# Kernel tuning notes

Measured on AMD Instinct MI355X. Metric: run time of the kernel, lower is better.

The kernel has to match this reference:

```python
import jax, jax.numpy as jnp
import numpy as np

N_DRUG, N_MICROBE = 1500, 1572
N = N_DRUG + N_MICROBE          # 3072 nodes
F_IN = 1546                     # raw feature dim (fc1: 1546 -> 256)
D0 = 256                        # GCN input dim after fc1
H1 = H2 = 128                   # GCN hidden dims (H1 + H2 = 256)
B = 16384                       # number of (left,right) query pairs


def _sym_norm(A):
    # D^{-1/2} A D^{-1/2} (no self loops), zeros kept for isolated nodes
    deg = A.sum(axis=1)
    d = jnp.where(deg > 0, jax.lax.rsqrt(deg), 0.0)
    return A * d[:, None] * d[None, :]


def _compute_inf(adj, L):
    # dl.compute_inf: L-hop influence = L-th power of sym-normalized adjacency
    An = _sym_norm(adj)
    M = An
    for _ in range(L - 1):
        M = M @ An
    return M


def _gcn_norm(W):
    # GCNConv normalization: add self loops (weight 1), sym-normalize by weighted degree
    Ahat = W + jnp.eye(W.shape[0], dtype=W.dtype)
    deg = Ahat.sum(axis=1)
    d = jnp.where(deg > 0, jax.lax.rsqrt(deg), 0.0)
    return Ahat * d[:, None] * d[None, :]


def _glorot(key, shape):
    return jax.random.normal(key, shape, dtype=jnp.float32) / np.sqrt(shape[0])


def setup_inputs() -> dict:
    key = jax.random.key(0)
    ks = jax.random.split(key, 24)
    u = jax.random.uniform(ks[0], (N, N), dtype=jnp.float32)
    w = jax.random.uniform(ks[1], (N, N), dtype=jnp.float32)
    adj = jnp.where(u < 0.01, w, 0.0)
    adj = jnp.maximum(adj, adj.T)
    X = jax.random.normal(ks[2], (N, F_IN), dtype=jnp.float32)
    left = jax.random.randint(ks[3], (B,), 0, N)
    right = jax.random.randint(ks[4], (B,), 0, N)
    return dict(
        left=left, right=right, X=X, adj=adj, threshold=jnp.float32(1e-4),
        W_fc1=_glorot(ks[5], (F_IN, D0)), b_fc1=jnp.zeros((D0,), jnp.float32),
        Wg1=_glorot(ks[6], (D0, H1)), bg1=jnp.zeros((H1,), jnp.float32),
        Wg2=_glorot(ks[7], (H1, H2)), bg2=jnp.zeros((H2,), jnp.float32),
        Wg3=_glorot(ks[8], (D0, H1)), bg3=jnp.zeros((H1,), jnp.float32),
        Wg4=_glorot(ks[9], (H1, H2)), bg4=jnp.zeros((H2,), jnp.float32),
        Wg5=_glorot(ks[10], (D0, H1)), bg5=jnp.zeros((H1,), jnp.float32),
        Wg6=_glorot(ks[11], (H1, H2)), bg6=jnp.zeros((H2,), jnp.float32),
        cnn_k=jax.random.normal(ks[12], (1, 3, 3, 3), dtype=jnp.float32) * 0.1,
        cnn_b=jnp.zeros((1,), jnp.float32),
        W_a=_glorot(ks[13], (2 * (H1 + H2), 64)), b_a=jnp.zeros((64,), jnp.float32),
        W_b=_glorot(ks[14], (64, 2)), b_b=jnp.zeros((2,), jnp.float32),
    )


def reference(left, right, X, adj, threshold,
              W_fc1, b_fc1, Wg1, bg1, Wg2, bg2, Wg3, bg3, Wg4, bg4,
              Wg5, bg5, Wg6, bg6, cnn_k, cnn_b, W_a, b_a, W_b, b_b):
    X0 = jax.nn.relu(X @ W_fc1 + b_fc1)  # fc1: [N, 1546] -> [N, 256]

    def branch(mask_src, Wa, ba, Wb, bb):
        # dynamically thresholded edges carry the ORIGINAL adj weights
        Wadj = jnp.where(mask_src > threshold, adj, 0.0)
        An = _gcn_norm(Wadj)                       # [N, N]
        e1 = jax.nn.relu(An @ (X0 @ Wa) + ba)      # GCNConv 1
        e2 = jax.nn.relu(An @ (e1 @ Wb) + bb)      # GCNConv 2
        return jnp.concatenate([e1, e2], axis=1)   # [N, 256]

    emb_l2 = branch(_compute_inf(adj, 2), Wg1, bg1, Wg2, bg2)
    emb_l1 = branch(_compute_inf(adj, 1), Wg3, bg3, Wg4, bg4)
    emb_l0 = branch(adj, Wg5, bg5, Wg6, bg6)

    emb = jnp.stack([emb_l0, emb_l1, emb_l2], axis=0)[None]  # [1, 3, N, 256]
    conv = jax.lax.conv_general_dilated(
        emb, cnn_k, window_strides=(1, 1), padding=[(2, 2), (2, 2)],
        rhs_dilation=(2, 2), dimension_numbers=('NCHW', 'OIHW', 'NCHW'))
    emb_all = conv[0, 0] + cnn_b[0]                # [N, 256]

    pair = jnp.concatenate([emb_all[left], emb_all[right]], axis=1)  # [B, 512]
    h = jax.nn.relu(pair @ W_a + b_a)              # dropout is identity at eval
    logits = h @ W_b + b_b                         # [B, 2]
    return logits, emb_all
```

## Files before the change

kernel.cpp:

```cpp
#include <hip/hip_runtime.h>

#define NN 3072
#define FIN 1546
#define KP 1568
#define MAXR 192

#define XS4_BLOCKS (NN * KP / 1024)
#define WSPLIT_BLOCKS (256 * KP / 256)
#define WG_BLOCKS 704
#define CSR_BLOCKS (NN / 4)
#define FC1_BLOCKS (NN / 16 * 4)

typedef __attribute__((ext_vector_type(8))) __bf16 bf16x8;
typedef __attribute__((ext_vector_type(4))) __bf16 bf16x4;
typedef __attribute__((ext_vector_type(4))) float f32x4;

__global__ __launch_bounds__(256) void prep_k(const float* __restrict__ adj,
                                              int* __restrict__ cols, float* __restrict__ vals,
                                              int* __restrict__ cnt, float* __restrict__ dvec,
                                              const float* __restrict__ X,
                                              __bf16* __restrict__ Xh, __bf16* __restrict__ Xl,
                                              const float* __restrict__ W,
                                              __bf16* __restrict__ WhT, __bf16* __restrict__ WlT,
                                              const float* __restrict__ Wga0,
                                              const float* __restrict__ Wga1,
                                              const float* __restrict__ Wga2,
                                              const float* __restrict__ Wgb0,
                                              const float* __restrict__ Wgb1,
                                              const float* __restrict__ Wgb2,
                                              const float* __restrict__ Wa,
                                              __bf16* __restrict__ WgaTh, __bf16* __restrict__ WgaTl,
                                              __bf16* __restrict__ WgbTh, __bf16* __restrict__ WgbTl,
                                              __bf16* __restrict__ WaTh, __bf16* __restrict__ WaTl) {
    int bid = blockIdx.x;
    if (bid < XS4_BLOCKS) {
        int e = (bid * 256 + threadIdx.x) * 4;
        int i = e / KP, c = e - i * KP;
        const float* xr = X + (size_t)i * FIN + c;
        float x0 = (c + 0 < FIN) ? xr[0] : 0.f;
        float x1 = (c + 1 < FIN) ? xr[1] : 0.f;
        float x2 = (c + 2 < FIN) ? xr[2] : 0.f;
        float x3 = (c + 3 < FIN) ? xr[3] : 0.f;
        __bf16 h0 = (__bf16)x0, h1 = (__bf16)x1, h2 = (__bf16)x2, h3 = (__bf16)x3;
        bf16x4 hv = {h0, h1, h2, h3};
        bf16x4 lv = {(__bf16)(x0 - (float)h0), (__bf16)(x1 - (float)h1),
                     (__bf16)(x2 - (float)h2), (__bf16)(x3 - (float)h3)};
        *(bf16x4*)(Xh + e) = hv;
        *(bf16x4*)(Xl + e) = lv;
        return;
    }
    bid -= XS4_BLOCKS;
    if (bid < WSPLIT_BLOCKS) {
        int idx = bid * 256 + threadIdx.x;
        int c = idx / KP, k = idx - c * KP;
        float x = (k < FIN) ? W[(size_t)k * 256 + c] : 0.f;
        __bf16 h = (__bf16)x;
        WhT[idx] = h;
        WlT[idx] = (__bf16)(x - (float)h);
        return;
    }
    bid -= WSPLIT_BLOCKS;
    if (bid < WG_BLOCKS) {
        int idx = bid * 256 + threadIdx.x;
        float x;
        __bf16 *oh, *ol;
        int off;
        if (idx < 98304) {
            int b = idx >> 15, r = idx & 32767;
            int c = r >> 8, k = r & 255;
            const float* Wp = (b == 0) ? Wga0 : (b == 1) ? Wga1 : Wga2;
            x = Wp[k * 128 + c];
            oh = WgaTh; ol = WgaTl; off = idx;
        } else if (idx < 98304 + 49152) {
            int j = idx - 98304;
            int b = j >> 14, r = j & 16383;
            int c = r >> 7, k = r & 127;
            const float* Wp = (b == 0) ? Wgb0 : (b == 1) ? Wgb1 : Wgb2;
            x = Wp[k * 128 + c];
            oh = WgbTh; ol = WgbTl; off = j;
        } else {
            int j = idx - 147456;
            int c = j >> 8, k = j & 255;
            x = (c < 64) ? Wa[(size_t)k * 64 + c] : Wa[(size_t)(256 + k) * 64 + (c - 64)];
            oh = WaTh; ol = WaTl; off = j;
        }
        __bf16 h = (__bf16)x;
        oh[off] = h;
        ol[off] = (__bf16)(x - (float)h);
        return;
    }
    bid -= WG_BLOCKS;
    int i = bid * 4 + (threadIdx.x >> 6);
    int lane = threadIdx.x & 63;
    const float* row = adj + (size_t)i * NN;
    unsigned long long below = (1ull << lane) - 1ull;
    float s = 0.f; int count = 0;
    int base = i * MAXR;
    for (int c0 = 0; c0 < NN; c0 += 256) {
        float4 a4 = *(const float4*)(row + c0 + lane * 4);
        float a[4] = {a4.x, a4.y, a4.z, a4.w};
        s += a[0] + a[1] + a[2] + a[3];
        unsigned long long bal[4];
        #pragma unroll
        for (int u = 0; u < 4; u++) bal[u] = __ballot(a[u] != 0.f);
        int before = 0;
        #pragma unroll
        for (int u = 0; u < 4; u++) before += __popcll(bal[u] & below);
        int local = 0;
        #pragma unroll
        for (int u = 0; u < 4; u++) {
            if (a[u] != 0.f) {
                int pos = count + before + local;
                if (pos < MAXR) { cols[base + pos] = c0 + lane * 4 + u; vals[base + pos] = a[u]; }
                local++;
            }
        }
        int tot = 0;
        #pragma unroll
        for (int u = 0; u < 4; u++) tot += __popcll(bal[u]);
        count += tot;
    }
    for (int off = 32; off; off >>= 1) s += __shfl_xor(s, off);
    if (lane == 0) {
        cnt[i] = count < MAXR ? count : MAXR;
        dvec[i] = (s > 0.f) ? 1.0f / sqrtf(s) : 0.f;
    }
}

__global__ __launch_bounds__(256) void fc1mask_k(const int* __restrict__ cols,
                                                 const float* __restrict__ vals,
                                                 const int* __restrict__ cnt,
                                                 const float* __restrict__ dvec,
                                                 const float* __restrict__ thrp,
                                                 int* __restrict__ mcols,
                                                 float* __restrict__ mvals,
                                                 int* __restrict__ mcnt,
                                                 float* __restrict__ db,
                                                 const __bf16* __restrict__ Xh,
                                                 const __bf16* __restrict__ Xl,
                                                 const __bf16* __restrict__ WhT,
                                                 const __bf16* __restrict__ WlT,
                                                 const float* __restrict__ bias,
                                                 __bf16* __restrict__ X0h,
                                                 __bf16* __restrict__ X0l) {
    __shared__ float ds[NN];
    __shared__ int lcols[MAXR];
    __shared__ float lvals[MAXR];
    __shared__ int lcnt;
    __shared__ float osum;
    int bid = blockIdx.x, tid = threadIdx.x;

    if (bid < FC1_BLOCKS) {
        int rt = bid >> 2;
        int c0 = (bid & 3) * 64;
        int w = tid >> 6, lane = tid & 63;
        int m = lane & 15, q = lane >> 4;
        int r0 = rt * 16;
        int cw = c0 + w * 16;
        const __bf16* xh = Xh + (size_t)(r0 + m) * KP + q * 8;
        const __bf16* xl = Xl + (size_t)(r0 + m) * KP + q * 8;
        const __bf16* bh = WhT + (size_t)(cw + m) * KP + q * 8;
        const __bf16* bl = WlT + (size_t)(cw + m) * KP + q * 8;

        f32x4 acc;
        #pragma unroll
        for (int r = 0; r < 4; r++) acc[r] = 0.f;

        #pragma unroll 7
        for (int ks = 0; ks < KP; ks += 32) {
            bf16x8 ah = *(const bf16x8*)(xh + ks);
            bf16x8 al = *(const bf16x8*)(xl + ks);
            bf16x8 bhv = *(const bf16x8*)(bh + ks);
            bf16x8 blv = *(const bf16x8*)(bl + ks);
            acc = __builtin_amdgcn_mfma_f32_16x16x32_bf16(ah, bhv, acc, 0, 0, 0);
            acc = __builtin_amdgcn_mfma_f32_16x16x32_bf16(ah, blv, acc, 0, 0, 0);
            acc = __builtin_amdgcn_mfma_f32_16x16x32_bf16(al, bhv, acc, 0, 0, 0);
        }
        int col = cw + m;
        float bv = bias[col];
        #pragma unroll
        for (int r = 0; r < 4; r++) {
            int row = r0 + q * 4 + r;
            float s = fmaxf(acc[r] + bv, 0.f);
            __bf16 h = (__bf16)s;
            X0h[(size_t)row * 256 + col] = h;
            X0l[(size_t)row * 256 + col] = (__bf16)(s - (float)h);
        }
        return;
    }

    int t = bid - FC1_BLOCKS;
    int mode, i;
    if (t < NN)          { mode = 2; i = t; }
    else if (t < 2 * NN) { mode = 0; i = t - NN; }
    else                 { mode = 1; i = t - 2 * NN; }

    mcols += (size_t)mode * NN * MAXR;
    mvals += (size_t)mode * NN * MAXR;
    mcnt  += (size_t)mode * NN;
    db    += (size_t)mode * NN;
    int ni = cnt[i], base = i * MAXR;
    float thr = *thrp;
    float di = dvec[i];

    if (mode < 2) {
        if (tid == 0) lcnt = 0;
        __syncthreads();
        float s = 0.f;
        if (tid < ni) {
            int j = cols[base + tid];
            float a = vals[base + tid];
            float m = (mode == 0) ? a : a * di * dvec[j];
            if (m > thr) {
                int p = atomicAdd(&lcnt, 1);
                mcols[base + p] = j;
                mvals[base + p] = a;
                s = a;
            }
        }
        ds[tid] = s; __syncthreads();
        for (int off = 128; off; off >>= 1) {
            if (tid < off) ds[tid] += ds[tid + off];
            __syncthreads();
        }
        if (tid == 0) {
            mcnt[i] = lcnt;
            db[i] = 1.0f / sqrtf(ds[0] + 1.0f);
        }
        return;
    }

    if (tid == 0) { osum = 0.f; lcnt = 0; }
    for (int j = tid; j < NN; j += 256) ds[j] = 0.f;
    __syncthreads();
    for (int t2 = tid; t2 < ni; t2 += 256) {
        int j = cols[base + t2];
        float a = vals[base + t2];
        lcols[t2] = j; lvals[t2] = a;
        ds[j] = a * dvec[j] * dvec[j];
    }
    __syncthreads();
    int lane = tid & 63, wv = tid >> 6;
    int sub = lane & 15, dg = lane >> 4;
    for (int o = wv * 4 + dg; o < ni; o += 16) {
        int j = lcols[o];
        int nj = cnt[j], bj = j * MAXR;
        float dot = 0.f;
        for (int t2 = sub; t2 < nj; t2 += 16)
            dot += vals[bj + t2] * ds[cols[bj + t2]];
        #pragma unroll
        for (int off = 8; off; off >>= 1) dot += __shfl_xor(dot, off);
        if (sub == 0 && di * dvec[j] * dot > thr) {
            int p = atomicAdd(&lcnt, 1);
            mcols[base + p] = j;
            mvals[base + p] = lvals[o];
            atomicAdd(&osum, lvals[o]);
        }
    }
    __syncthreads();
    if (tid == 0) {
        mcnt[i] = lcnt;
        db[i] = 1.0f / sqrtf(osum + 1.0f);
    }
}

__global__ __launch_bounds__(256) void gemm3m_k(const __bf16* __restrict__ Ah,
                                                const __bf16* __restrict__ Al,
                                                int aplane, int K,
                                                const __bf16* __restrict__ Bh,
                                                const __bf16* __restrict__ Bl,
                                                float* __restrict__ out) {
    int tid = threadIdx.x;
    int w = tid >> 6, lane = tid & 63;
    int m = lane & 15, q = lane >> 4;
    int i0 = blockIdx.x * 64, c0 = blockIdx.y * 64;
    int z = blockIdx.z;
    int rowA = i0 + w * 16 + m;
    const __bf16* ah = Ah + (size_t)z * aplane + (size_t)rowA * K + q * 8;
    const __bf16* al = Al + (size_t)z * aplane + (size_t)rowA * K + q * 8;
    const __bf16* bh0 = Bh + (size_t)z * 128 * K + (size_t)(c0 + m) * K + q * 8;
    const __bf16* bl0 = Bl + (size_t)z * 128 * K + (size_t)(c0 + m) * K + q * 8;

    f32x4 acc[4];
    #pragma unroll
    for (int ct = 0; ct < 4; ct++)
        #pragma unroll
        for (int r = 0; r < 4; r++) acc[ct][r] = 0.f;

    for (int ks = 0; ks < K; ks += 32) {
        bf16x8 a_h = *(const bf16x8*)(ah + ks);
        bf16x8 a_l = *(const bf16x8*)(al + ks);
        #pragma unroll
        for (int ct = 0; ct < 4; ct++) {
            bf16x8 b_h = *(const bf16x8*)(bh0 + (size_t)ct * 16 * K + ks);
            bf16x8 b_l = *(const bf16x8*)(bl0 + (size_t)ct * 16 * K + ks);
            acc[ct] = __builtin_amdgcn_mfma_f32_16x16x32_bf16(a_h, b_h, acc[ct], 0, 0, 0);
            acc[ct] = __builtin_amdgcn_mfma_f32_16x16x32_bf16(a_h, b_l, acc[ct], 0, 0, 0);
            acc[ct] = __builtin_amdgcn_mfma_f32_16x16x32_bf16(a_l, b_h, acc[ct], 0, 0, 0);
        }
    }
    float* outp = out + (size_t)z * NN * 128;
    int rowBase = i0 + w * 16 + q * 4;
    #pragma unroll
    for (int ct = 0; ct < 4; ct++) {
        int col = c0 + ct * 16 + m;
        #pragma unroll
        for (int r = 0; r < 4; r++)
            outp[(size_t)(rowBase + r) * 128 + col] = acc[ct][r];
    }
}

__global__ __launch_bounds__(256) void spmm3_k(const int* __restrict__ mcols,
                                               const float* __restrict__ mvals,
                                               const int* __restrict__ mcnt,
                                               const float* __restrict__ db,
                                               const float* __restrict__ Xin,
                                               const float* __restrict__ bias0,
                                               const float* __restrict__ bias1,
                                               const float* __restrict__ bias2,
                                               __bf16* __restrict__ outAh,
                                               __bf16* __restrict__ outAl,
                                               float* __restrict__ embf, int coff) {
    __shared__ float lcoef[MAXR];
    __shared__ int lj[MAXR];
    __shared__ float4 part[8][32];
    int i = blockIdx.x, tid = threadIdx.x, b = blockIdx.y;
    mcols += (size_t)b * NN * MAXR;
    mvals += (size_t)b * NN * MAXR;
    mcnt  += (size_t)b * NN;
    db    += (size_t)b * NN;
    const float* Xb = Xin + (size_t)b * NN * 128;
    const float* bias = (b == 0) ? bias0 : (b == 1) ? bias1 : bias2;
    float dbi = db[i];
    int n = mcnt[i], base = i * MAXR;
    if (tid < n) {
        int j = mcols[base + tid];
        lj[tid] = j;
        lcoef[tid] = mvals[base + tid] * dbi * db[j];
    }
    __syncthreads();
    int g = tid >> 5, c4 = (tid & 31) << 2;
    float4 acc = make_float4(0.f, 0.f, 0.f, 0.f);
    float4 acc2 = make_float4(0.f, 0.f, 0.f, 0.f);
    if (g == 0) {
        float4 x = *(const float4*)&Xb[(size_t)i * 128 + c4];
        float d2 = dbi * dbi;
        acc = make_float4(d2 * x.x, d2 * x.y, d2 * x.z, d2 * x.w);
    }
    int t = g;
    for (; t + 8 < n; t += 16) {
        float cf0 = lcoef[t];
        float4 x0 = *(const float4*)&Xb[(size_t)lj[t] * 128 + c4];
        float cf1 = lcoef[t + 8];
        float4 x1 = *(const float4*)&Xb[(size_t)lj[t + 8] * 128 + c4];
        acc.x += cf0 * x0.x; acc.y += cf0 * x0.y; acc.z += cf0 * x0.z; acc.w += cf0 * x0.w;
        acc2.x += cf1 * x1.x; acc2.y += cf1 * x1.y; acc2.z += cf1 * x1.z; acc2.w += cf1 * x1.w;
    }
    if (t < n) {
        float cf = lcoef[t];
        float4 x = *(const float4*)&Xb[(size_t)lj[t] * 128 + c4];
        acc.x += cf * x.x; acc.y += cf * x.y; acc.z += cf * x.z; acc.w += cf * x.w;
    }
    acc.x += acc2.x; acc.y += acc2.y; acc.z += acc2.z; acc.w += acc2.w;
    part[g][tid & 31] = acc;
    __syncthreads();
    if (tid < 32) {
        float4 s = part[0][tid];
        #pragma unroll
        for (int gg = 1; gg < 8; gg++) {
            float4 t4 = part[gg][tid];
            s.x += t4.x; s.y += t4.y; s.z += t4.z; s.w += t4.w;
        }
        int cc = tid << 2;
        float4 bv = *(const float4*)&bias[cc];
        s.x = fmaxf(s.x + bv.x, 0.f); s.y = fmaxf(s.y + bv.y, 0.f);
        s.z = fmaxf(s.z + bv.z, 0.f); s.w = fmaxf(s.w + bv.w, 0.f);
        if (outAh) {
            __bf16 h0 = (__bf16)s.x, h1 = (__bf16)s.y, h2 = (__bf16)s.z, h3 = (__bf16)s.w;
            bf16x4 hv = {h0, h1, h2, h3};
            bf16x4 lv = {(__bf16)(s.x - (float)h0), (__bf16)(s.y - (float)h1),
                         (__bf16)(s.z - (float)h2), (__bf16)(s.w - (float)h3)};
            *(bf16x4*)(outAh + ((size_t)b * NN + i) * 128 + cc) = hv;
            *(bf16x4*)(outAl + ((size_t)b * NN + i) * 128 + cc) = lv;
        }
        *(float4*)&embf[((size_t)b * NN + i) * 256 + coff + cc] = s;
    }
}

__global__ __launch_bounds__(256) void conv3f_k(const float* __restrict__ emb,
                                                const float* __restrict__ ck,
                                                const float* __restrict__ cb,
                                                float* __restrict__ outf,
                                                __bf16* __restrict__ embh,
                                                __bf16* __restrict__ embl) {
    __shared__ float rows[3][3][256];
    int n = blockIdx.x, c = threadIdx.x;
    #pragma unroll
    for (int i = 0; i < 3; i++)
        #pragma unroll
        for (int kh = 0; kh < 3; kh++) {
            int nn2 = n + 2 * kh - 2;
            rows[i][kh][c] = (nn2 >= 0 && nn2 < NN) ? emb[((size_t)i * NN + nn2) * 256 + c] : 0.f;
        }
    __syncthreads();
    float s = cb[0];
    #pragma unroll
    for (int i = 0; i < 3; i++)
        #pragma unroll
        for (int kh = 0; kh < 3; kh++)
            #pragma unroll
            for (int kw = 0; kw < 3; kw++) {
                int cc = c + 2 * kw - 2;
                if (cc >= 0 && cc < 256)
                    s += rows[i][kh][cc] * ck[(i * 3 + kh) * 3 + kw];
            }
    size_t idx = (size_t)n * 256 + c;
    outf[idx] = s;
    __bf16 h = (__bf16)s;
    embh[idx] = h;
    embl[idx] = (__bf16)(s - (float)h);
}

__global__ __launch_bounds__(256) void gemmuvm_k(const __bf16* __restrict__ Ah,
                                                 const __bf16* __restrict__ Al,
                                                 const __bf16* __restrict__ Bh,
                                                 const __bf16* __restrict__ Bl,
                                                 float* __restrict__ uvp) {
    int tid = threadIdx.x;
    int w = tid >> 6, lane = tid & 63;
    int m = lane & 15, q = lane >> 4;
    int i0 = blockIdx.x * 64, c0 = blockIdx.y * 64;
    int rowA = i0 + w * 16 + m;
    const __bf16* ah = Ah + (size_t)rowA * 256 + q * 8;
    const __bf16* al = Al + (size_t)rowA * 256 + q * 8;
    const __bf16* bh0 = Bh + (size_t)(c0 + m) * 256 + q * 8;
    const __bf16* bl0 = Bl + (size_t)(c0 + m) * 256 + q * 8;

    f32x4 acc[4];
    #pragma unroll
    for (int ct = 0; ct < 4; ct++)
        #pragma unroll
        for (int r = 0; r < 4; r++) acc[ct][r] = 0.f;

    for (int ks = 0; ks < 256; ks += 32) {
        bf16x8 a_h = *(const bf16x8*)(ah + ks);
        bf16x8 a_l = *(const bf16x8*)(al + ks);
        #pragma unroll
        for (int ct = 0; ct < 4; ct++) {
            bf16x8 b_h = *(const bf16x8*)(bh0 + (size_t)ct * 16 * 256 + ks);
            bf16x8 b_l = *(const bf16x8*)(bl0 + (size_t)ct * 16 * 256 + ks);
            acc[ct] = __builtin_amdgcn_mfma_f32_16x16x32_bf16(a_h, b_h, acc[ct], 0, 0, 0);
            acc[ct] = __builtin_amdgcn_mfma_f32_16x16x32_bf16(a_h, b_l, acc[ct], 0, 0, 0);
            acc[ct] = __builtin_amdgcn_mfma_f32_16x16x32_bf16(a_l, b_h, acc[ct], 0, 0, 0);
        }
    }
    int rowBase = i0 + w * 16 + q * 4;
    #pragma unroll
    for (int ct = 0; ct < 4; ct++) {
        int col = c0 + ct * 16 + m;
        #pragma unroll
        for (int r = 0; r < 4; r++)
            uvp[(size_t)(rowBase + r) * 128 + col] = acc[ct][r];
    }
}

__global__ __launch_bounds__(256) void pairuv_k(const int* __restrict__ left,
                                                const int* __restrict__ right,
                                                const float* __restrict__ uvp,
                                                const float* __restrict__ ba,
                                                const float* __restrict__ Wb,
                                                const float* __restrict__ bb,
                                                float* __restrict__ out) {
    int tid = threadIdx.x;
    int w = tid >> 6, c = tid & 63;
    int base = blockIdx.x * 16 + w * 4;
    float bac = ba[c];
    float w0 = Wb[c * 2], w1 = Wb[c * 2 + 1];
    float b0 = bb[0], b1 = bb[1];
    #pragma unroll
    for (int pp = 0; pp < 4; pp++) {
        int row = base + pp;
        int l = left[row], r = right[row];
        float h = uvp[(size_t)l * 128 + c] + uvp[(size_t)r * 128 + 64 + c] + bac;
        h = fmaxf(h, 0.f);
        float s0 = h * w0, s1 = h * w1;
        for (int off = 32; off; off >>= 1) {
            s0 += __shfl_xor(s0, off);
            s1 += __shfl_xor(s1, off);
        }
        if (c == 0) {
            out[row * 2]     = s0 + b0;
            out[row * 2 + 1] = s1 + b1;
        }
    }
}

extern "C" void kernel_launch(void* const* d_in, const int* in_sizes, int n_in,
                              void* d_out, int out_size, void* d_ws, size_t ws_size,
                              hipStream_t stream) {
    const int* left  = (const int*)d_in[0];
    const int* right = (const int*)d_in[1];
    const float* X    = (const float*)d_in[2];
    const float* adj  = (const float*)d_in[3];
    const float* thr  = (const float*)d_in[4];
    const float* Wfc1 = (const float*)d_in[5];
    const float* bfc1 = (const float*)d_in[6];
    const float* Wga[3] = { (const float*)d_in[15], (const float*)d_in[11], (const float*)d_in[7] };
    const float* bga[3] = { (const float*)d_in[16], (const float*)d_in[12], (const float*)d_in[8] };
    const float* Wgb[3] = { (const float*)d_in[17], (const float*)d_in[13], (const float*)d_in[9] };
    const float* bgb[3] = { (const float*)d_in[18], (const float*)d_in[14], (const float*)d_in[10] };
    const float* cnnk = (const float*)d_in[19];
    const float* cnnb = (const float*)d_in[20];
    const float* Wa_  = (const float*)d_in[21];
    const float* ba_  = (const float*)d_in[22];
    const float* Wb_  = (const float*)d_in[23];
    const float* bb_  = (const float*)d_in[24];

    char* p = (char*)d_ws;
    auto take = [&](size_t n) { char* q = p; p += (n + 255) & ~(size_t)255; return q; };
    float* dvec = (float*)take(NN * 4);
    float* db3  = (float*)take((size_t)3 * NN * 4);
    int*   cnt  = (int*)take(NN * 4);
    int*   mcnt3 = (int*)take((size_t)3 * NN * 4);
    int*   cols = (int*)take((size_t)NN * MAXR * 4);
    float* vals = (float*)take((size_t)NN * MAXR * 4);
    int*   mcols3 = (int*)take((size_t)3 * NN * MAXR * 4);
    float* mvals3 = (float*)take((size_t)3 * NN * MAXR * 4);
    __bf16* X0h  = (__bf16*)take((size_t)NN * 256 * 2);
    __bf16* X0l  = (__bf16*)take((size_t)NN * 256 * 2);
    float* XWall = (float*)take((size_t)3 * NN * 128 * 4);
    __bf16* e1h  = (__bf16*)take((size_t)3 * NN * 128 * 2);
    __bf16* e1l  = (__bf16*)take((size_t)3 * NN * 128 * 2);
    float* HW2all= (float*)take((size_t)3 * NN * 128 * 4);
    float* embf  = (float*)take((size_t)3 * NN * 256 * 4);
    __bf16* Xh   = (__bf16*)take((size_t)NN * KP * 2);
    __bf16* Xl   = (__bf16*)take((size_t)NN * KP * 2);
    __bf16* WhT  = (__bf16*)take((size_t)256 * KP * 2);
    __bf16* WlT  = (__bf16*)take((size_t)256 * KP * 2);
    __bf16* WgaTh = (__bf16*)take((size_t)3 * 128 * 256 * 2);
    __bf16* WgaTl = (__bf16*)take((size_t)3 * 128 * 256 * 2);
    __bf16* WgbTh = (__bf16*)take((size_t)3 * 128 * 128 * 2);
    __bf16* WgbTl = (__bf16*)take((size_t)3 * 128 * 128 * 2);
    __bf16* WaTh  = (__bf16*)take((size_t)128 * 256 * 2);
    __bf16* WaTl  = (__bf16*)take((size_t)128 * 256 * 2);
    __bf16* embh  = (__bf16*)take((size_t)NN * 256 * 2);
    __bf16* embl  = (__bf16*)take((size_t)NN * 256 * 2);
    float* uvp   = (float*)take((size_t)NN * 128 * 4);

    float* out_logits = (float*)d_out;
    float* out_emb = out_logits + 32768;

    prep_k<<<XS4_BLOCKS + WSPLIT_BLOCKS + WG_BLOCKS + CSR_BLOCKS, 256, 0, stream>>>(
        adj, cols, vals, cnt, dvec, X, Xh, Xl, Wfc1, WhT, WlT,
        Wga[0], Wga[1], Wga[2], Wgb[0], Wgb[1], Wgb[2], Wa_,
        WgaTh, WgaTl, WgbTh, WgbTl, WaTh, WaTl);

    fc1mask_k<<<FC1_BLOCKS + 3 * NN, 256, 0, stream>>>(cols, vals, cnt, dvec, thr,
                                                       mcols3, mvals3, mcnt3, db3,
                                                       Xh, Xl, WhT, WlT, bfc1, X0h, X0l);

    gemm3m_k<<<dim3(NN / 64, 2, 3), 256, 0, stream>>>(X0h, X0l, 0, 256, WgaTh, WgaTl, XWall);
    spmm3_k<<<dim3(NN, 3), 256, 0, stream>>>(mcols3, mvals3, mcnt3, db3, XWall,
                                             bga[0], bga[1], bga[2], e1h, e1l, embf, 0);
    gemm3m_k<<<dim3(NN / 64, 2, 3), 256, 0, stream>>>(e1h, e1l, NN * 128, 128, WgbTh, WgbTl, HW2all);
    spmm3_k<<<dim3(NN, 3), 256, 0, stream>>>(mcols3, mvals3, mcnt3, db3, HW2all,
                                             bgb[0], bgb[1], bgb[2], (__bf16*)0, (__bf16*)0, embf, 128);

    conv3f_k<<<NN, 256, 0, stream>>>(embf, cnnk, cnnb, out_emb, embh, embl);
    gemmuvm_k<<<dim3(NN / 64, 2), 256, 0, stream>>>(embh, embl, WaTh, WaTl, uvp);
    pairuv_k<<<16384 / 16, 256, 0, stream>>>(left, right, uvp, ba_, Wb_, bb_, out_logits);
}
```

Baseline: 303.5 us.

## Fuse small GEMMs into SpMM and conv epilogues and regroup prep kernels

```diff
diff --git a/kernel.cpp b/kernel.cpp
--- a/kernel.cpp
+++ b/kernel.cpp
@@ -7,7 +7,7 @@
 
 #define XS4_BLOCKS (NN * KP / 1024)
 #define WSPLIT_BLOCKS (256 * KP / 256)
-#define WG_BLOCKS 704
+#define WGA_BLOCKS 384
 #define CSR_BLOCKS (NN / 4)
 #define FC1_BLOCKS (NN / 16 * 4)
 
@@ -15,23 +15,14 @@
 typedef __attribute__((ext_vector_type(4))) __bf16 bf16x4;
 typedef __attribute__((ext_vector_type(4))) float f32x4;
 
-__global__ __launch_bounds__(256) void prep_k(const float* __restrict__ adj,
-                                              int* __restrict__ cols, float* __restrict__ vals,
-                                              int* __restrict__ cnt, float* __restrict__ dvec,
-                                              const float* __restrict__ X,
-                                              __bf16* __restrict__ Xh, __bf16* __restrict__ Xl,
-                                              const float* __restrict__ W,
-                                              __bf16* __restrict__ WhT, __bf16* __restrict__ WlT,
-                                              const float* __restrict__ Wga0,
-                                              const float* __restrict__ Wga1,
-                                              const float* __restrict__ Wga2,
-                                              const float* __restrict__ Wgb0,
-                                              const float* __restrict__ Wgb1,
-                                              const float* __restrict__ Wgb2,
-                                              const float* __restrict__ Wa,
-                                              __bf16* __restrict__ WgaTh, __bf16* __restrict__ WgaTl,
-                                              __bf16* __restrict__ WgbTh, __bf16* __restrict__ WgbTl,
-                                              __bf16* __restrict__ WaTh, __bf16* __restrict__ WaTl) {
+__global__ __launch_bounds__(256) void prep1_k(const float* __restrict__ X,
+                                               __bf16* __restrict__ Xh, __bf16* __restrict__ Xl,
+                                               const float* __restrict__ W,
+                                               __bf16* __restrict__ WhT, __bf16* __restrict__ WlT,
+                                               const float* __restrict__ Wga0,
+                                               const float* __restrict__ Wga1,
+                                               const float* __restrict__ Wga2,
+                                               __bf16* __restrict__ WgaTh, __bf16* __restrict__ WgaTl) {
     int bid = blockIdx.x;
     if (bid < XS4_BLOCKS) {
         int e = (bid * 256 + threadIdx.x) * 4;
@@ -60,96 +51,27 @@
         return;
     }
     bid -= WSPLIT_BLOCKS;
-    if (bid < WG_BLOCKS) {
-        int idx = bid * 256 + threadIdx.x;
-        float x;
-        __bf16 *oh, *ol;
-        int off;
-        if (idx < 98304) {
-            int b = idx >> 15, r = idx & 32767;
-            int c = r >> 8, k = r & 255;
-            const float* Wp = (b == 0) ? Wga0 : (b == 1) ? Wga1 : Wga2;
-            x = Wp[k * 128 + c];
-            oh = WgaTh; ol = WgaTl; off = idx;
-        } else if (idx < 98304 + 49152) {
-            int j = idx - 98304;
-            int b = j >> 14, r = j & 16383;
-            int c = r >> 7, k = r & 127;
-            const float* Wp = (b == 0) ? Wgb0 : (b == 1) ? Wgb1 : Wgb2;
-            x = Wp[k * 128 + c];
-            oh = WgbTh; ol = WgbTl; off = j;
-        } else {
-            int j = idx - 147456;
-            int c = j >> 8, k = j & 255;
-            x = (c < 64) ? Wa[(size_t)k * 64 + c] : Wa[(size_t)(256 + k) * 64 + (c - 64)];
-            oh = WaTh; ol = WaTl; off = j;
-        }
-        __bf16 h = (__bf16)x;
-        oh[off] = h;
-        ol[off] = (__bf16)(x - (float)h);
-        return;
-    }
-    bid -= WG_BLOCKS;
-    int i = bid * 4 + (threadIdx.x >> 6);
-    int lane = threadIdx.x & 63;
-    const float* row = adj + (size_t)i * NN;
-    unsigned long long below = (1ull << lane) - 1ull;
-    float s = 0.f; int count = 0;
-    int base = i * MAXR;
-    for (int c0 = 0; c0 < NN; c0 += 256) {
-        float4 a4 = *(const float4*)(row + c0 + lane * 4);
-        float a[4] = {a4.x, a4.y, a4.z, a4.w};
-        s += a[0] + a[1] + a[2] + a[3];
-        unsigned long long bal[4];
-        #pragma unroll
-        for (int u = 0; u < 4; u++) bal[u] = __ballot(a[u] != 0.f);
-        int before = 0;
-        #pragma unroll
-        for (int u = 0; u < 4; u++) before += __popcll(bal[u] & below);
-        int local = 0;
-        #pragma unroll
-        for (int u = 0; u < 4; u++) {
-            if (a[u] != 0.f) {
-                int pos = count + before + local;
-                if (pos < MAXR) { cols[base + pos] = c0 + lane * 4 + u; vals[base + pos] = a[u]; }
-                local++;
-            }
-        }
-        int tot = 0;
-        #pragma unroll
-        for (int u = 0; u < 4; u++) tot += __popcll(bal[u]);
-        count += tot;
-    }
-    for (int off = 32; off; off >>= 1) s += __shfl_xor(s, off);
-    if (lane == 0) {
-        cnt[i] = count < MAXR ? count : MAXR;
-        dvec[i] = (s > 0.f) ? 1.0f / sqrtf(s) : 0.f;
-    }
-}
-
-__global__ __launch_bounds__(256) void fc1mask_k(const int* __restrict__ cols,
-                                                 const float* __restrict__ vals,
-                                                 const int* __restrict__ cnt,
-                                                 const float* __restrict__ dvec,
-                                                 const float* __restrict__ thrp,
-                                                 int* __restrict__ mcols,
-                                                 float* __restrict__ mvals,
-                                                 int* __restrict__ mcnt,
-                                                 float* __restrict__ db,
-                                                 const __bf16* __restrict__ Xh,
-                                                 const __bf16* __restrict__ Xl,
-                                                 const __bf16* __restrict__ WhT,
-                                                 const __bf16* __restrict__ WlT,
-                                                 const float* __restrict__ bias,
-                                                 __bf16* __restrict__ X0h,
-                                                 __bf16* __restrict__ X0l) {
-    __shared__ float ds[NN];
-    __shared__ int lcols[MAXR];
-    __shared__ float lvals[MAXR];
-    __shared__ int lcnt;
-    __shared__ float osum;
+    int idx = bid * 256 + threadIdx.x;
+    int b = idx >> 15, r = idx & 32767;
+    int c = r >> 8, k = r & 255;
+    const float* Wp = (b == 0) ? Wga0 : (b == 1) ? Wga1 : Wga2;
+    float x = Wp[k * 128 + c];
+    __bf16 h = (__bf16)x;
+    WgaTh[idx] = h;
+    WgaTl[idx] = (__bf16)(x - (float)h);
+}
+
+__global__ __launch_bounds__(256) void fc1csr_k(const float* __restrict__ adj,
+                                                int* __restrict__ cols, float* __restrict__ vals,
+                                                int* __restrict__ cnt, float* __restrict__ dvec,
+                                                const __bf16* __restrict__ Xh,
+                                                const __bf16* __restrict__ Xl,
+                                                const __bf16* __restrict__ WhT,
+                                                const __bf16* __restrict__ WlT,
+                                                const float* __restrict__ bias,
+                                                __bf16* __restrict__ X0h,
+                                                __bf16* __restrict__ X0l) {
     int bid = blockIdx.x, tid = threadIdx.x;
-
     if (bid < FC1_BLOCKS) {
         int rt = bid >> 2;
         int c0 = (bid & 3) * 64;
@@ -188,8 +110,107 @@
         }
         return;
     }
-
-    int t = bid - FC1_BLOCKS;
+    int i = (bid - FC1_BLOCKS) * 4 + (tid >> 6);
+    int lane = tid & 63;
+    const float* row = adj + (size_t)i * NN;
+    unsigned long long below = (1ull << lane) - 1ull;
+    float s = 0.f; int count = 0;
+    int base = i * MAXR;
+    for (int c0 = 0; c0 < NN; c0 += 256) {
+        float4 a4 = *(const float4*)(row + c0 + lane * 4);
+        float a[4] = {a4.x, a4.y, a4.z, a4.w};
+        s += a[0] + a[1] + a[2] + a[3];
+        unsigned long long bal[4];
+        #pragma unroll
+        for (int u = 0; u < 4; u++) bal[u] = __ballot(a[u] != 0.f);
+        int before = 0;
+        #pragma unroll
+        for (int u = 0; u < 4; u++) before += __popcll(bal[u] & below);
+        int local = 0;
+        #pragma unroll
+        for (int u = 0; u < 4; u++) {
+            if (a[u] != 0.f) {
+                int pos = count + before + local;
+                if (pos < MAXR) { cols[base + pos] = c0 + lane * 4 + u; vals[base + pos] = a[u]; }
+                local++;
+            }
+        }
+        int tot = 0;
+        #pragma unroll
+        for (int u = 0; u < 4; u++) tot += __popcll(bal[u]);
+        count += tot;
+    }
+    for (int off = 32; off; off >>= 1) s += __shfl_xor(s, off);
+    if (lane == 0) {
+        cnt[i] = count < MAXR ? count : MAXR;
+        dvec[i] = (s > 0.f) ? 1.0f / sqrtf(s) : 0.f;
+    }
+}
+
+__global__ __launch_bounds__(256) void maskg1_k(const int* __restrict__ cols,
+                                                const float* __restrict__ vals,
+                                                const int* __restrict__ cnt,
+                                                const float* __restrict__ dvec,
+                                                const float* __restrict__ thrp,
+                                                int* __restrict__ mcols,
+                                                float* __restrict__ mvals,
+                                                int* __restrict__ mcnt,
+                                                float* __restrict__ db,
+                                                const __bf16* __restrict__ X0h,
+                                                const __bf16* __restrict__ X0l,
+                                                const __bf16* __restrict__ WgaTh,
+                                                const __bf16* __restrict__ WgaTl,
+                                                float* __restrict__ XWall) {
+    __shared__ float ds[NN];
+    __shared__ int lcols[MAXR];
+    __shared__ float lvals[MAXR];
+    __shared__ int lcnt;
+    __shared__ float osum;
+    int bid = blockIdx.x, tid = threadIdx.x;
+
+    if (bid >= 3 * NN) {
+        int g = bid - 3 * NN;
+        int bx = g % 48, by = (g / 48) & 1, bz = g / 96;
+        int w = tid >> 6, lane = tid & 63;
+        int m = lane & 15, q = lane >> 4;
+        int i0 = bx * 64, c0 = by * 64;
+        int rowA = i0 + w * 16 + m;
+        const __bf16* ah = X0h + (size_t)rowA * 256 + q * 8;
+        const __bf16* al = X0l + (size_t)rowA * 256 + q * 8;
+        const __bf16* bh0 = WgaTh + (size_t)bz * 128 * 256 + (size_t)(c0 + m) * 256 + q * 8;
+        const __bf16* bl0 = WgaTl + (size_t)bz * 128 * 256 + (size_t)(c0 + m) * 256 + q * 8;
+
+        f32x4 acc[4];
+        #pragma unroll
+        for (int ct = 0; ct < 4; ct++)
+            #pragma unroll
+            for (int r = 0; r < 4; r++) acc[ct][r] = 0.f;
+
+        for (int ks = 0; ks < 256; ks += 32) {
+            bf16x8 a_h = *(const bf16x8*)(ah + ks);
+            bf16x8 a_l = *(const bf16x8*)(al + ks);
+            #pragma unroll
+            for (int ct = 0; ct < 4; ct++) {
+                bf16x8 b_h = *(const bf16x8*)(bh0 + (size_t)ct * 16 * 256 + ks);
+                bf16x8 b_l = *(const bf16x8*)(bl0 + (size_t)ct * 16 * 256 + ks);
+                acc[ct] = __builtin_amdgcn_mfma_f32_16x16x32_bf16(a_h, b_h, acc[ct], 0, 0, 0);
+                acc[ct] = __builtin_amdgcn_mfma_f32_16x16x32_bf16(a_h, b_l, acc[ct], 0, 0, 0);
+                acc[ct] = __builtin_amdgcn_mfma_f32_16x16x32_bf16(a_l, b_h, acc[ct], 0, 0, 0);
+            }
+        }
+        float* outp = XWall + (size_t)bz * NN * 128;
+        int rowBase = i0 + w * 16 + q * 4;
+        #pragma unroll
+        for (int ct = 0; ct < 4; ct++) {
+            int col = c0 + ct * 16 + m;
+            #pragma unroll
+            for (int r = 0; r < 4; r++)
+                outp[(size_t)(rowBase + r) * 128 + col] = acc[ct][r];
+        }
+        return;
+    }
+
+    int t = bid;
     int mode, i;
     if (t < NN)          { mode = 2; i = t; }
     else if (t < 2 * NN) { mode = 0; i = t - NN; }
@@ -241,15 +262,15 @@
     }
     __syncthreads();
     int lane = tid & 63, wv = tid >> 6;
-    int sub = lane & 15, dg = lane >> 4;
-    for (int o = wv * 4 + dg; o < ni; o += 16) {
+    int sub = lane & 7, dg = lane >> 3;
+    for (int o = wv * 8 + dg; o < ni; o += 32) {
         int j = lcols[o];
         int nj = cnt[j], bj = j * MAXR;
         float dot = 0.f;
-        for (int t2 = sub; t2 < nj; t2 += 16)
+        for (int t2 = sub; t2 < nj; t2 += 8)
             dot += vals[bj + t2] * ds[cols[bj + t2]];
         #pragma unroll
-        for (int off = 8; off; off >>= 1) dot += __shfl_xor(dot, off);
+        for (int off = 4; off; off >>= 1) dot += __shfl_xor(dot, off);
         if (sub == 0 && di * dvec[j] * dot > thr) {
             int p = atomicAdd(&lcnt, 1);
             mcols[base + p] = j;
@@ -261,52 +282,6 @@
     if (tid == 0) {
         mcnt[i] = lcnt;
         db[i] = 1.0f / sqrtf(osum + 1.0f);
-    }
-}
-
-__global__ __launch_bounds__(256) void gemm3m_k(const __bf16* __restrict__ Ah,
-                                                const __bf16* __restrict__ Al,
-                                                int aplane, int K,
-                                                const __bf16* __restrict__ Bh,
-                                                const __bf16* __restrict__ Bl,
-                                                float* __restrict__ out) {
-    int tid = threadIdx.x;
-    int w = tid >> 6, lane = tid & 63;
-    int m = lane & 15, q = lane >> 4;
-    int i0 = blockIdx.x * 64, c0 = blockIdx.y * 64;
-    int z = blockIdx.z;
-    int rowA = i0 + w * 16 + m;
-    const __bf16* ah = Ah + (size_t)z * aplane + (size_t)rowA * K + q * 8;
-    const __bf16* al = Al + (size_t)z * aplane + (size_t)rowA * K + q * 8;
-    const __bf16* bh0 = Bh + (size_t)z * 128 * K + (size_t)(c0 + m) * K + q * 8;
-    const __bf16* bl0 = Bl + (size_t)z * 128 * K + (size_t)(c0 + m) * K + q * 8;
-
-    f32x4 acc[4];
-    #pragma unroll
-    for (int ct = 0; ct < 4; ct++)
-        #pragma unroll
-        for (int r = 0; r < 4; r++) acc[ct][r] = 0.f;
-
-    for (int ks = 0; ks < K; ks += 32) {
-        bf16x8 a_h = *(const bf16x8*)(ah + ks);
-        bf16x8 a_l = *(const bf16x8*)(al + ks);
-        #pragma unroll
-        for (int ct = 0; ct < 4; ct++) {
-            bf16x8 b_h = *(const bf16x8*)(bh0 + (size_t)ct * 16 * K + ks);
-            bf16x8 b_l = *(const bf16x8*)(bl0 + (size_t)ct * 16 * K + ks);
-            acc[ct] = __builtin_amdgcn_mfma_f32_16x16x32_bf16(a_h, b_h, acc[ct], 0, 0, 0);
-            acc[ct] = __builtin_amdgcn_mfma_f32_16x16x32_bf16(a_h, b_l, acc[ct], 0, 0, 0);
-            acc[ct] = __builtin_amdgcn_mfma_f32_16x16x32_bf16(a_l, b_h, acc[ct], 0, 0, 0);
-        }
-    }
-    float* outp = out + (size_t)z * NN * 128;
-    int rowBase = i0 + w * 16 + q * 4;
-    #pragma unroll
-    for (int ct = 0; ct < 4; ct++) {
-        int col = c0 + ct * 16 + m;
-        #pragma unroll
-        for (int r = 0; r < 4; r++)
-            outp[(size_t)(rowBase + r) * 128 + col] = acc[ct][r];
     }
 }
 
@@ -318,12 +293,16 @@
                                                const float* __restrict__ bias0,
                                                const float* __restrict__ bias1,
                                                const float* __restrict__ bias2,
-                                               __bf16* __restrict__ outAh,
-                                               __bf16* __restrict__ outAl,
-                                               float* __restrict__ embf, int coff) {
+                                               float* __restrict__ embf, int coff,
+                                               const float* __restrict__ Wgb0,
+                                               const float* __restrict__ Wgb1,
+                                               const float* __restrict__ Wgb2,
+                                               float* __restrict__ HW2out) {
     __shared__ float lcoef[MAXR];
     __shared__ int lj[MAXR];
     __shared__ float4 part[8][32];
+    __shared__ float e1row[128];
+    __shared__ float part2[2][128];
     int i = blockIdx.x, tid = threadIdx.x, b = blockIdx.y;
     mcols += (size_t)b * NN * MAXR;
     mvals += (size_t)b * NN * MAXR;
@@ -375,25 +354,34 @@
         float4 bv = *(const float4*)&bias[cc];
         s.x = fmaxf(s.x + bv.x, 0.f); s.y = fmaxf(s.y + bv.y, 0.f);
         s.z = fmaxf(s.z + bv.z, 0.f); s.w = fmaxf(s.w + bv.w, 0.f);
-        if (outAh) {
-            __bf16 h0 = (__bf16)s.x, h1 = (__bf16)s.y, h2 = (__bf16)s.z, h3 = (__bf16)s.w;
-            bf16x4 hv = {h0, h1, h2, h3};
-            bf16x4 lv = {(__bf16)(s.x - (float)h0), (__bf16)(s.y - (float)h1),
-                         (__bf16)(s.z - (float)h2), (__bf16)(s.w - (float)h3)};
-            *(bf16x4*)(outAh + ((size_t)b * NN + i) * 128 + cc) = hv;
-            *(bf16x4*)(outAl + ((size_t)b * NN + i) * 128 + cc) = lv;
-        }
         *(float4*)&embf[((size_t)b * NN + i) * 256 + coff + cc] = s;
-    }
-}
-
-__global__ __launch_bounds__(256) void conv3f_k(const float* __restrict__ emb,
+        *(float4*)&e1row[cc] = s;
+    }
+    if (!HW2out) return;
+    __syncthreads();
+    int o = tid & 127, h = tid >> 7;
+    const float* Wg = (b == 0) ? Wgb0 : (b == 1) ? Wgb1 : Wgb2;
+    float ha = 0.f;
+    int kbase = h * 64;
+    const float* wp = Wg + (size_t)kbase * 128 + o;
+    #pragma unroll 8
+    for (int kk = 0; kk < 64; kk++)
+        ha += e1row[kbase + kk] * wp[(size_t)kk * 128];
+    part2[h][o] = ha;
+    __syncthreads();
+    if (tid < 128)
+        HW2out[((size_t)b * NN + i) * 128 + tid] = part2[0][tid] + part2[1][tid];
+}
+
+__global__ __launch_bounds__(256) void convuv_k(const float* __restrict__ emb,
                                                 const float* __restrict__ ck,
                                                 const float* __restrict__ cb,
                                                 float* __restrict__ outf,
-                                                __bf16* __restrict__ embh,
-                                                __bf16* __restrict__ embl) {
+                                                const float* __restrict__ Wa,
+                                                float* __restrict__ uvp) {
     __shared__ float rows[3][3][256];
+    __shared__ float embrow[256];
+    __shared__ float part2[2][128];
     int n = blockIdx.x, c = threadIdx.x;
     #pragma unroll
     for (int i = 0; i < 3; i++)
@@ -416,52 +404,20 @@
             }
     size_t idx = (size_t)n * 256 + c;
     outf[idx] = s;
-    __bf16 h = (__bf16)s;
-    embh[idx] = h;
-    embl[idx] = (__bf16)(s - (float)h);
-}
-
-__global__ __launch_bounds__(256) void gemmuvm_k(const __bf16* __restrict__ Ah,
-                                                 const __bf16* __restrict__ Al,
-                                                 const __bf16* __restrict__ Bh,
-                                                 const __bf16* __restrict__ Bl,
-                                                 float* __restrict__ uvp) {
-    int tid = threadIdx.x;
-    int w = tid >> 6, lane = tid & 63;
-    int m = lane & 15, q = lane >> 4;
-    int i0 = blockIdx.x * 64, c0 = blockIdx.y * 64;
-    int rowA = i0 + w * 16 + m;
-    const __bf16* ah = Ah + (size_t)rowA * 256 + q * 8;
-    const __bf16* al = Al + (size_t)rowA * 256 + q * 8;
-    const __bf16* bh0 = Bh + (size_t)(c0 + m) * 256 + q * 8;
-    const __bf16* bl0 = Bl + (size_t)(c0 + m) * 256 + q * 8;
-
-    f32x4 acc[4];
-    #pragma unroll
-    for (int ct = 0; ct < 4; ct++)
-        #pragma unroll
-        for (int r = 0; r < 4; r++) acc[ct][r] = 0.f;
-
-    for (int ks = 0; ks < 256; ks += 32) {
-        bf16x8 a_h = *(const bf16x8*)(ah + ks);
-        bf16x8 a_l = *(const bf16x8*)(al + ks);
-        #pragma unroll
-        for (int ct = 0; ct < 4; ct++) {
-            bf16x8 b_h = *(const bf16x8*)(bh0 + (size_t)ct * 16 * 256 + ks);
-            bf16x8 b_l = *(const bf16x8*)(bl0 + (size_t)ct * 16 * 256 + ks);
-            acc[ct] = __builtin_amdgcn_mfma_f32_16x16x32_bf16(a_h, b_h, acc[ct], 0, 0, 0);
-            acc[ct] = __builtin_amdgcn_mfma_f32_16x16x32_bf16(a_h, b_l, acc[ct], 0, 0, 0);
-            acc[ct] = __builtin_amdgcn_mfma_f32_16x16x32_bf16(a_l, b_h, acc[ct], 0, 0, 0);
-        }
-    }
-    int rowBase = i0 + w * 16 + q * 4;
-    #pragma unroll
-    for (int ct = 0; ct < 4; ct++) {
-        int col = c0 + ct * 16 + m;
-        #pragma unroll
-        for (int r = 0; r < 4; r++)
-            uvp[(size_t)(rowBase + r) * 128 + col] = acc[ct][r];
-    }
+    embrow[c] = s;
+    __syncthreads();
+    int o = c & 127, h = c >> 7;
+    int kbase = h * 128;
+    const float* wp = (o < 64) ? (Wa + (size_t)kbase * 64 + o)
+                               : (Wa + (size_t)(256 + kbase) * 64 + (o - 64));
+    float acc = 0.f;
+    #pragma unroll 8
+    for (int kk = 0; kk < 128; kk++)
+        acc += embrow[kbase + kk] * wp[(size_t)kk * 64];
+    part2[h][o] = acc;
+    __syncthreads();
+    if (c < 128)
+        uvp[(size_t)n * 128 + c] = part2[0][c] + part2[1][c];
 }
 
 __global__ __launch_bounds__(256) void pairuv_k(const int* __restrict__ left,
@@ -529,8 +485,6 @@
     __bf16* X0h  = (__bf16*)take((size_t)NN * 256 * 2);
     __bf16* X0l  = (__bf16*)take((size_t)NN * 256 * 2);
     float* XWall = (float*)take((size_t)3 * NN * 128 * 4);
-    __bf16* e1h  = (__bf16*)take((size_t)3 * NN * 128 * 2);
-    __bf16* e1l  = (__bf16*)take((size_t)3 * NN * 128 * 2);
     float* HW2all= (float*)take((size_t)3 * NN * 128 * 4);
     float* embf  = (float*)take((size_t)3 * NN * 256 * 4);
     __bf16* Xh   = (__bf16*)take((size_t)NN * KP * 2);
@@ -539,34 +493,31 @@
     __bf16* WlT  = (__bf16*)take((size_t)256 * KP * 2);
     __bf16* WgaTh = (__bf16*)take((size_t)3 * 128 * 256 * 2);
     __bf16* WgaTl = (__bf16*)take((size_t)3 * 128 * 256 * 2);
-    __bf16* WgbTh = (__bf16*)take((size_t)3 * 128 * 128 * 2);
-    __bf16* WgbTl = (__bf16*)take((size_t)3 * 128 * 128 * 2);
-    __bf16* WaTh  = (__bf16*)take((size_t)128 * 256 * 2);
-    __bf16* WaTl  = (__bf16*)take((size_t)128 * 256 * 2);
-    __bf16* embh  = (__bf16*)take((size_t)NN * 256 * 2);
-    __bf16* embl  = (__bf16*)take((size_t)NN * 256 * 2);
     float* uvp   = (float*)take((size_t)NN * 128 * 4);
 
     float* out_logits = (float*)d_out;
     float* out_emb = out_logits + 32768;
 
-    prep_k<<<XS4_BLOCKS + WSPLIT_BLOCKS + WG_BLOCKS + CSR_BLOCKS, 256, 0, stream>>>(
-        adj, cols, vals, cnt, dvec, X, Xh, Xl, Wfc1, WhT, WlT,
-        Wga[0], Wga[1], Wga[2], Wgb[0], Wgb[1], Wgb[2], Wa_,
-        WgaTh, WgaTl, WgbTh, WgbTl, WaTh, WaTl);
-
-    fc1mask_k<<<FC1_BLOCKS + 3 * NN, 256, 0, stream>>>(cols, vals, cnt, dvec, thr,
-                                                       mcols3, mvals3, mcnt3, db3,
-                                                       Xh, Xl, WhT, WlT, bfc1, X0h, X0l);
-
-    gemm3m_k<<<dim3(NN / 64, 2, 3), 256, 0, stream>>>(X0h, X0l, 0, 256, WgaTh, WgaTl, XWall);
+    prep1_k<<<XS4_BLOCKS + WSPLIT_BLOCKS + WGA_BLOCKS, 256, 0, stream>>>(
+        X, Xh, Xl, Wfc1, WhT, WlT, Wga[0], Wga[1], Wga[2], WgaTh, WgaTl);
+
+    fc1csr_k<<<FC1_BLOCKS + CSR_BLOCKS, 256, 0, stream>>>(
+        adj, cols, vals, cnt, dvec, Xh, Xl, WhT, WlT, bfc1, X0h, X0l);
+
+    maskg1_k<<<3 * NN + 288, 256, 0, stream>>>(cols, vals, cnt, dvec, thr,
+                                               mcols3, mvals3, mcnt3, db3,
+                                               X0h, X0l, WgaTh, WgaTl, XWall);
+
     spmm3_k<<<dim3(NN, 3), 256, 0, stream>>>(mcols3, mvals3, mcnt3, db3, XWall,
-                                             bga[0], bga[1], bga[2], e1h, e1l, embf, 0);
-    gemm3m_k<<<dim3(NN / 64, 2, 3), 256, 0, stream>>>(e1h, e1l, NN * 128, 128, WgbTh, WgbTl, HW2all);
+                                             bga[0], bga[1], bga[2], embf, 0,
+                                             Wgb[0], Wgb[1], Wgb[2], HW2all);
+
     spmm3_k<<<dim3(NN, 3), 256, 0, stream>>>(mcols3, mvals3, mcnt3, db3, HW2all,
-                                             bgb[0], bgb[1], bgb[2], (__bf16*)0, (__bf16*)0, embf, 128);
-
-    conv3f_k<<<NN, 256, 0, stream>>>(embf, cnnk, cnnb, out_emb, embh, embl);
-    gemmuvm_k<<<dim3(NN / 64, 2), 256, 0, stream>>>(embh, embl, WaTh, WaTl, uvp);
+                                             bgb[0], bgb[1], bgb[2], embf, 128,
+                                             (const float*)0, (const float*)0, (const float*)0,
+                                             (float*)0);
+
+    convuv_k<<<NN, 256, 0, stream>>>(embf, cnnk, cnnb, out_emb, Wa_, uvp);
+
     pairuv_k<<<16384 / 16, 256, 0, stream>>>(left, right, uvp, ba_, Wb_, bb_, out_logits);
 }
```

Result: slower. 322.9 us (+6.4%).
